# Performance work log

Measured on AMD Instinct MI355X. Metric: run time of the kernel, lower is better.

## Reference

```python
import jax, jax.numpy as jnp
import numpy as np

N_NODES = 100000
N_EDGES = 1600000
IN_DIM, HID, OUT_DIM = 128, 128, 64


def _glorot(key, fan_in, fan_out):
    s = float(np.sqrt(6.0 / (fan_in + fan_out)))
    return jax.random.uniform(key, (fan_in, fan_out), jnp.float32, -s, s)


def setup_inputs() -> dict:
    key = jax.random.key(0)
    ks = jax.random.split(key, 6)
    x = jax.random.normal(ks[0], (N_NODES, IN_DIM), jnp.float32)
    edge_index = jax.random.randint(ks[1], (2, N_EDGES), 0, N_NODES, jnp.int32)
    return {
        "x": x,
        "edge_index": edge_index,
        "W0": _glorot(ks[2], IN_DIM, HID), "b0": jnp.zeros((HID,), jnp.float32),
        "W1": _glorot(ks[3], HID, HID),    "b1": jnp.zeros((HID,), jnp.float32),
        "W2": _glorot(ks[4], HID, OUT_DIM), "b2": jnp.zeros((OUT_DIM,), jnp.float32),
    }


def _gcn_conv(x, src, dst, norm, W, b):
    # x' = D^{-1/2} (A+I) D^{-1/2} X W + b  (PyG GCNConv, add_self_loops=True)
    h = x @ W                       # [N, F_out]
    msg = h[src] * norm[:, None]    # [E+N, F_out] gathered, normalized messages
    out = jax.ops.segment_sum(msg, dst, num_segments=x.shape[0])
    return out + b


def reference(x, edge_index, W0, b0, W1, b1, W2, b2):
    n = x.shape[0]
    loop = jnp.arange(n, dtype=edge_index.dtype)
    src = jnp.concatenate([edge_index[0], loop])  # self-loops appended
    dst = jnp.concatenate([edge_index[1], loop])
    deg = jax.ops.segment_sum(jnp.ones_like(src, jnp.float32), dst, num_segments=n)
    dis = jnp.where(deg > 0, jax.lax.rsqrt(jnp.maximum(deg, 1e-12)), 0.0)
    norm = dis[src] * dis[dst]      # symmetric GCN normalization per edge

    h = jax.nn.relu(_gcn_conv(x, src, dst, norm, W0, b0))
    h = jax.nn.relu(_gcn_conv(h, src, dst, norm, W1, b1))
    h = jax.nn.relu(_gcn_conv(h, src, dst, norm, W2, b2))
    return jax.nn.log_softmax(h, axis=1)
```

## Files before the change

kernel.cpp:

```cpp
#include <hip/hip_runtime.h>

#define NN 100000
#define NE 1600000
#define NBK 782
#define NBLK 256
#define CHUNK ((NE + NBLK - 1) / NBLK)

typedef __bf16 bf16x4 __attribute__((ext_vector_type(4)));
typedef __bf16 bf16x8 __attribute__((ext_vector_type(8)));
typedef float f32x2 __attribute__((ext_vector_type(2)));
typedef float f32x4 __attribute__((ext_vector_type(4)));

#define ACC8_FP8(vv)                                                                  \
  {                                                                                   \
    f32x2 p;                                                                          \
    p = __builtin_amdgcn_cvt_pk_f32_fp8((vv).x, 0); acc[0] += p[0]; acc[1] += p[1];   \
    p = __builtin_amdgcn_cvt_pk_f32_fp8((vv).x, 1); acc[2] += p[0]; acc[3] += p[1];   \
    p = __builtin_amdgcn_cvt_pk_f32_fp8((vv).y, 0); acc[4] += p[0]; acc[5] += p[1];   \
    p = __builtin_amdgcn_cvt_pk_f32_fp8((vv).y, 1); acc[6] += p[0]; acc[7] += p[1];   \
  }


__global__ __launch_bounds__(256) void kW_prep(const float* __restrict__ W0, const float* __restrict__ W1,
                                               const float* __restrict__ W2, __bf16* __restrict__ Wt) {
  int i = blockIdx.x * 256 + threadIdx.x;
  if (i < 16384) {
    int k = i >> 7, n = i & 127;
    Wt[n * 128 + k] = (__bf16)W0[i];
  } else if (i < 32768) {
    int j = i - 16384;
    int k = j >> 7, n = j & 127;
    Wt[16384 + n * 128 + k] = (__bf16)W1[j];
  } else if (i < 40960) {
    int j = i - 32768;
    int k = j >> 6, n = j & 63;
    Wt[32768 + n * 128 + k] = (__bf16)W2[j];
  }
}


__global__ __launch_bounds__(256) void k1_hist(const int* __restrict__ dst, int* __restrict__ bhist) {
  __shared__ int h[NBK];
  int tid = threadIdx.x, b = blockIdx.x;
  for (int i = tid; i < NBK; i += 256) h[i] = 0;
  __syncthreads();
  int base = b * CHUNK, end = min(base + CHUNK, NE);
  for (int e = base + tid; e < end; e += 256) atomicAdd(&h[dst[e] >> 7], 1);
  __syncthreads();
  for (int i = tid; i < NBK; i += 256) bhist[i * NBLK + b] = h[i];
}

__global__ __launch_bounds__(256) void kA2(const int* __restrict__ bhist, int* __restrict__ btot) {
  int w = threadIdx.x >> 6, lane = threadIdx.x & 63;
  int bin = blockIdx.x * 4 + w;
  if (bin >= NBK) return;
  int4 v = *(const int4*)(bhist + bin * NBLK + lane * 4);
  int s = v.x + v.y + v.z + v.w;
#pragma unroll
  for (int off = 32; off > 0; off >>= 1) s += __shfl_xor(s, off);
  if (lane == 0) btot[bin] = s;
}

__global__ __launch_bounds__(1024) void kB_bscan(const int* __restrict__ btot, int* __restrict__ bptr) {
  __shared__ int s[1024];
  int tid = threadIdx.x;
  int v = (tid < NBK) ? btot[tid] : 0;
  s[tid] = v;
  __syncthreads();
  for (int off = 1; off < 1024; off <<= 1) {
    int t = (tid >= off) ? s[tid - off] : 0;
    __syncthreads();
    s[tid] += t;
    __syncthreads();
  }
  if (tid < NBK) bptr[tid + 1] = s[tid];
  if (tid == 0) bptr[0] = 0;
}

__global__ __launch_bounds__(256) void kC2(const int* __restrict__ bhist, const int* __restrict__ bptr,
                                           int* __restrict__ blockbase) {
  int w = threadIdx.x >> 6, lane = threadIdx.x & 63;
  int bin = blockIdx.x * 4 + w;
  if (bin >= NBK) return;
  int4 v = *(const int4*)(bhist + bin * NBLK + lane * 4);
  int ls = v.x + v.y + v.z + v.w;
  int incl = ls;
#pragma unroll
  for (int off = 1; off < 64; off <<= 1) {
    int t = __shfl_up(incl, off);
    if (lane >= off) incl += t;
  }
  int base = bptr[bin] + incl - ls;
  int4 o;
  o.x = base;
  o.y = base + v.x;
  o.z = base + v.x + v.y;
  o.w = base + v.x + v.y + v.z;
  *(int4*)(blockbase + bin * NBLK + lane * 4) = o;
}

__global__ __launch_bounds__(256) void k3_scatter(const int* __restrict__ src, const int* __restrict__ dst,
                                                  const int* __restrict__ blockbase, int* __restrict__ bucketed) {
  __shared__ int cur[NBK];
  int tid = threadIdx.x, b = blockIdx.x;
  for (int i = tid; i < NBK; i += 256) cur[i] = blockbase[i * NBLK + b];
  __syncthreads();
  int base = b * CHUNK, end = min(base + CHUNK, NE);
  for (int e = base + tid; e < end; e += 256) {
    int d = dst[e];
    int pos = atomicAdd(&cur[d >> 7], 1);
    bucketed[pos] = (src[e] << 7) | (d & 127);
  }
}

__global__ __launch_bounds__(256) void k_degfill(const int* __restrict__ bucketed, const int* __restrict__ bptr,
                                                 int* __restrict__ row_ptr, float* __restrict__ dis,
                                                 int* __restrict__ csr_src) {
  __shared__ int deg[128];
  __shared__ int sc[128];
  __shared__ int cur[128];
  int b = blockIdx.x, tid = threadIdx.x;
  int nb0 = b << 7;
  if (tid < 128) deg[tid] = 0;
  __syncthreads();
  int beg = bptr[b], end = bptr[b + 1];
  for (int e = beg + tid; e < end; e += 256) atomicAdd(&deg[bucketed[e] & 127], 1);
  __syncthreads();
  if (tid < 128) sc[tid] = deg[tid];
  __syncthreads();
  for (int off = 1; off < 128; off <<= 1) {
    int t = (tid >= off && tid < 128) ? sc[tid - off] : 0;
    __syncthreads();
    if (tid < 128) sc[tid] += t;
    __syncthreads();
  }
  if (tid < 128) {
    cur[tid] = beg + sc[tid] - deg[tid];
    if (nb0 + tid < NN) {
      row_ptr[nb0 + tid + 1] = beg + sc[tid];
      dis[nb0 + tid] = rsqrtf((float)(deg[tid] + 1));
      if (b == 0 && tid == 0) row_ptr[0] = 0;
    }
  }
  __syncthreads();
  for (int e = beg + tid; e < end; e += 256) {
    int pk = bucketed[e];
    int pos = atomicAdd(&cur[pk & 127], 1);
    csr_src[pos] = pk >> 7;
  }
}


template <int BN, int MODE, bool OUT8>
__global__ __launch_bounds__(256) void k_gemm(const void* __restrict__ Av, const __bf16* __restrict__ Wt,
                                              const float* __restrict__ bias, const float* __restrict__ dis,
                                              void* __restrict__ outv) {
  constexpr int LDK = 136;
  constexpr int NT = BN / 32;
  constexpr int ROWB = BN * (OUT8 ? 1 : 2);
  __shared__ __bf16 lB[BN * LDK];

  const int tid = threadIdx.x;
  const int rowBase = blockIdx.x * 128;
  const int lane = tid & 63;
  const int wid = tid >> 6;
  const int wm = (wid & 1) * 64;
  const int wn = (wid >> 1) * (BN / 2);
  const int lm = lane & 15;
  const int kg = lane >> 4;

  if (blockIdx.x == 0 && tid < ROWB / 16) {
    ((uint4*)((char*)outv + (size_t)NN * ROWB))[tid] = make_uint4(0, 0, 0, 0);
  }

  for (int c = tid; c < 16 * BN; c += 256) {
    int n = c >> 4;
    int koff = (c & 15) * 8;
    bf16x8 w = *(const bf16x8*)(Wt + n * 128 + koff);
    *(bf16x8*)&lB[n * LDK + koff] = w;
  }
  __syncthreads();

  f32x4 acc[4][NT] = {};
  const bool full = (rowBase + 128 <= NN);

#pragma unroll 2
  for (int ks = 0; ks < 128; ks += 32) {
    int k0 = ks + kg * 8;
    bf16x8 af[4];
    if constexpr (MODE == 0) {
      const float* A = (const float*)Av;
#pragma unroll
      for (int tm = 0; tm < 4; ++tm) {
        int gr = rowBase + wm + tm * 16 + lm;
        f32x4 a0 = {}, a1 = {};
        if (full || gr < NN) {
          a0 = *(const f32x4*)(A + (size_t)gr * 128 + k0);
          a1 = *(const f32x4*)(A + (size_t)gr * 128 + k0 + 4);
        }
        af[tm] = bf16x8{(__bf16)a0[0], (__bf16)a0[1], (__bf16)a0[2], (__bf16)a0[3],
                        (__bf16)a1[0], (__bf16)a1[1], (__bf16)a1[2], (__bf16)a1[3]};
      }
    } else {
      const __bf16* A = (const __bf16*)Av;
      f32x4 b0 = *(const f32x4*)(bias + k0);
      f32x4 b1 = *(const f32x4*)(bias + k0 + 4);
#pragma unroll
      for (int tm = 0; tm < 4; ++tm) {
        int gr = rowBase + wm + tm * 16 + lm;
        bf16x8 v = {};
        if (full || gr < NN) v = *(const bf16x8*)(A + (size_t)gr * 128 + k0);
        af[tm] = bf16x8{(__bf16)fmaxf((float)v[0] + b0[0], 0.f), (__bf16)fmaxf((float)v[1] + b0[1], 0.f),
                        (__bf16)fmaxf((float)v[2] + b0[2], 0.f), (__bf16)fmaxf((float)v[3] + b0[3], 0.f),
                        (__bf16)fmaxf((float)v[4] + b1[0], 0.f), (__bf16)fmaxf((float)v[5] + b1[1], 0.f),
                        (__bf16)fmaxf((float)v[6] + b1[2], 0.f), (__bf16)fmaxf((float)v[7] + b1[3], 0.f)};
      }
    }
    bf16x8 bfr[NT];
#pragma unroll
    for (int tn = 0; tn < NT; ++tn)
      bfr[tn] = *(const bf16x8*)&lB[(wn + tn * 16 + lm) * LDK + k0];
#pragma unroll
    for (int tm = 0; tm < 4; ++tm)
#pragma unroll
      for (int tn = 0; tn < NT; ++tn)
        acc[tm][tn] = __builtin_amdgcn_mfma_f32_16x16x32_bf16(af[tm], bfr[tn], acc[tm][tn], 0, 0, 0);
  }

#pragma unroll
  for (int tm = 0; tm < 4; ++tm) {
    int r0 = rowBase + wm + tm * 16 + kg * 4;
#pragma unroll
    for (int tn = 0; tn < NT; ++tn) {
      int c0 = wn + tn * 16 + lm;
#pragma unroll
      for (int r = 0; r < 4; ++r) {
        int gr = r0 + r;
        if (full || gr < NN) {
          float val = acc[tm][tn][r] * dis[gr];
          if constexpr (OUT8) {
            unsigned char* o8 = (unsigned char*)outv;
            unsigned pk = __builtin_amdgcn_cvt_pk_fp8_f32(val, val, 0, 0);
            o8[(size_t)gr * BN + c0] = (unsigned char)(pk & 0xffu);
          } else {
            __bf16* ob = (__bf16*)outv;
            ob[(size_t)gr * BN + c0] = (__bf16)val;
          }
        }
      }
    }
  }
}


__global__ __launch_bounds__(256) void k_agg128(const unsigned char* __restrict__ tmp8, const int* __restrict__ row_ptr,
                                                const int* __restrict__ csr_src, const float* __restrict__ dis,
                                                __bf16* __restrict__ agg) {
  int wid = (blockIdx.x * 256 + threadIdx.x) >> 6;
  int lane = threadIdx.x & 63;
  if (wid >= NN) return;
  int grp = lane >> 4;
  int fl = lane & 15;

  int beg = row_ptr[wid];
  int end = row_ptr[wid + 1];

  float acc[8] = {0.f, 0.f, 0.f, 0.f, 0.f, 0.f, 0.f, 0.f};
  if (grp == 0) {
    uint2 sv = *(const uint2*)(tmp8 + (size_t)wid * 128 + fl * 8);
    ACC8_FP8(sv);
  }

  for (int base = beg; base < end; base += 64) {
    int cnt = min(64, end - base);
    int sidx = (base + lane < end) ? csr_src[base + lane] : NN;
    int i = 0;
    while (i < cnt) {
      int rem = cnt - i;
      if (rem > 16) {
        uint2 v[8];
#pragma unroll
        for (int u = 0; u < 8; ++u) {
          int s = __shfl(sidx, (i + u * 4 + grp) & 63);
          v[u] = *(const uint2*)(tmp8 + (size_t)s * 128 + fl * 8);
        }
#pragma unroll
        for (int u = 0; u < 8; ++u) ACC8_FP8(v[u]);
        i += 32;
      } else {
        uint2 v[4];
#pragma unroll
        for (int u = 0; u < 4; ++u) {
          int s = __shfl(sidx, (i + u * 4 + grp) & 63);
          v[u] = *(const uint2*)(tmp8 + (size_t)s * 128 + fl * 8);
        }
#pragma unroll
        for (int u = 0; u < 4; ++u) ACC8_FP8(v[u]);
        i += 16;
      }
    }
  }

#pragma unroll
  for (int t = 0; t < 8; ++t) acc[t] += __shfl_xor(acc[t], 16);
#pragma unroll
  for (int t = 0; t < 8; ++t) acc[t] += __shfl_xor(acc[t], 32);

  if (grp == 0) {
    float d = dis[wid];
    bf16x8 o;
#pragma unroll
    for (int t = 0; t < 8; ++t) o[t] = (__bf16)(acc[t] * d);
    *(bf16x8*)&agg[(size_t)wid * 128 + fl * 8] = o;
  }
}


__global__ __launch_bounds__(256) void k_agg64_final(const __bf16* __restrict__ tmp, const int* __restrict__ row_ptr,
                                                     const int* __restrict__ csr_src, const float* __restrict__ dis,
                                                     const float* __restrict__ b2, float* __restrict__ out) {
  int wid = (blockIdx.x * 256 + threadIdx.x) >> 6;
  int lane = threadIdx.x & 63;
  int grp = lane >> 4;
  int fl = lane & 15;

  int beg = row_ptr[wid];
  int end = row_ptr[wid + 1];

  float acc[4] = {0.f, 0.f, 0.f, 0.f};
  if (grp == 0) {
    bf16x4 sv = *(const bf16x4*)&tmp[(size_t)wid * 64 + fl * 4];
#pragma unroll
    for (int t = 0; t < 4; ++t) acc[t] = (float)sv[t];
  }

  for (int base = beg; base < end; base += 64) {
    int cnt = min(64, end - base);
    int sidx = (base + lane < end) ? csr_src[base + lane] : NN;
    int i = 0;
    while (i < cnt) {
      int rem = cnt - i;
      if (rem > 16) {
        bf16x4 v[8];
#pragma unroll
        for (int u = 0; u < 8; ++u) {
          int s = __shfl(sidx, (i + u * 4 + grp) & 63);
          v[u] = *(const bf16x4*)&tmp[(size_t)s * 64 + fl * 4];
        }
#pragma unroll
        for (int u = 0; u < 8; ++u)
#pragma unroll
          for (int t = 0; t < 4; ++t) acc[t] += (float)v[u][t];
        i += 32;
      } else {
        bf16x4 v[4];
#pragma unroll
        for (int u = 0; u < 4; ++u) {
          int s = __shfl(sidx, (i + u * 4 + grp) & 63);
          v[u] = *(const bf16x4*)&tmp[(size_t)s * 64 + fl * 4];
        }
#pragma unroll
        for (int u = 0; u < 4; ++u)
#pragma unroll
          for (int t = 0; t < 4; ++t) acc[t] += (float)v[u][t];
        i += 16;
      }
    }
  }

#pragma unroll
  for (int t = 0; t < 4; ++t) acc[t] += __shfl_xor(acc[t], 16);
#pragma unroll
  for (int t = 0; t < 4; ++t) acc[t] += __shfl_xor(acc[t], 32);

  float d = dis[wid];
  float v[4], lm = -1e30f;
#pragma unroll
  for (int t = 0; t < 4; ++t) {
    v[t] = fmaxf(acc[t] * d + b2[fl * 4 + t], 0.f);
    lm = fmaxf(lm, v[t]);
  }
#pragma unroll
  for (int off = 8; off > 0; off >>= 1) lm = fmaxf(lm, __shfl_xor(lm, off));
  float le = 0.f;
#pragma unroll
  for (int t = 0; t < 4; ++t) le += __expf(v[t] - lm);
#pragma unroll
  for (int off = 8; off > 0; off >>= 1) le += __shfl_xor(le, off);
  float ls = lm + __logf(le);
  if (grp == 0) {
    f32x4 o = {v[0] - ls, v[1] - ls, v[2] - ls, v[3] - ls};
    *(f32x4*)&out[(size_t)wid * 64 + fl * 4] = o;
  }
}


extern "C" void kernel_launch(void* const* d_in, const int* in_sizes, int n_in,
                              void* d_out, int out_size, void* d_ws, size_t ws_size,
                              hipStream_t stream) {
  const float* x  = (const float*)d_in[0];
  const int*   ei = (const int*)d_in[1];
  const float* W0 = (const float*)d_in[2];
  const float* b0 = (const float*)d_in[3];
  const float* W1 = (const float*)d_in[4];
  const float* b1 = (const float*)d_in[5];
  const float* W2 = (const float*)d_in[6];
  const float* b2 = (const float*)d_in[7];
  const int* esrc = ei;
  const int* edst = ei + NE;

  char* p = (char*)d_ws;
  auto alloc = [&](size_t bytes) {
    char* q = p;
    p += (bytes + 255) & ~(size_t)255;
    return q;
  };
  float*  dis     = (float*)alloc((size_t)NN * 4);
  int*    row_ptr = (int*)alloc((size_t)(NN + 1) * 4);
  int*    btot    = (int*)alloc(NBK * 4);
  int*    bptr    = (int*)alloc((NBK + 1) * 4);
  __bf16* Wt      = (__bf16*)alloc(40960 * 2);
  int*    csr_src = (int*)alloc((size_t)NE * 4);
  char*   tmp     = (char*)alloc((size_t)(NN + 1) * 128 * 2);
  unsigned char* tmp8 = (unsigned char*)tmp;
  __bf16* tmp16   = (__bf16*)tmp;
  int*    bucketed  = (int*)tmp;
  int*    bhist     = csr_src;
  int*    blockbase = csr_src + NBLK * NBK;

  kW_prep<<<160, 256, 0, stream>>>(W0, W1, W2, Wt);
  k1_hist<<<NBLK, 256, 0, stream>>>(edst, bhist);
  kA2<<<(NBK + 3) / 4, 256, 0, stream>>>(bhist, btot);
  kB_bscan<<<1, 1024, 0, stream>>>(btot, bptr);
  kC2<<<(NBK + 3) / 4, 256, 0, stream>>>(bhist, bptr, blockbase);
  k3_scatter<<<NBLK, 256, 0, stream>>>(esrc, edst, blockbase, bucketed);
  k_degfill<<<NBK, 256, 0, stream>>>(bucketed, bptr, row_ptr, dis, csr_src);

  int gblocks = (NN + 127) / 128;
  int ablocks = (NN * 64 + 255) / 256;

  k_gemm<128, 0, true><<<gblocks, 256, 0, stream>>>(x, Wt, nullptr, dis, tmp8);
  k_agg128<<<ablocks, 256, 0, stream>>>(tmp8, row_ptr, csr_src, dis, (__bf16*)d_out);

  k_gemm<128, 2, true><<<gblocks, 256, 0, stream>>>(d_out, Wt + 16384, b0, dis, tmp8);
  k_agg128<<<ablocks, 256, 0, stream>>>(tmp8, row_ptr, csr_src, dis, (__bf16*)d_out);

  k_gemm<64, 2, false><<<gblocks, 256, 0, stream>>>(d_out, Wt + 32768, b1, dis, tmp16);
  k_agg64_final<<<ablocks, 256, 0, stream>>>(tmp16, row_ptr, csr_src, dis, b2, (float*)d_out);
}
```

Baseline: 364.0 us.

## Map four nodes per wavefront in aggregation, fuse weight prep, use warp-shuffle scan

The aggregation kernels now give each 16-lane group of a wavefront its own destination node instead of spreading one node's edges across four groups. This removes the cross-group shuffle reductions and launches a quarter as many blocks. The cost is that every group in a wavefront loops to the largest degree among its four nodes, so lanes go idle when degrees differ. Weight transposition is folded into extra blocks of the histogram kernel to save a launch, and the block-offset scan now uses wave shuffles instead of a barrier-heavy shared-memory scan.

```diff
diff --git a/kernel.cpp b/kernel.cpp
--- a/kernel.cpp
+++ b/kernel.cpp
@@ -21,27 +21,28 @@
   }
 
 
-__global__ __launch_bounds__(256) void kW_prep(const float* __restrict__ W0, const float* __restrict__ W1,
+__global__ __launch_bounds__(256) void k1_hist(const int* __restrict__ dst, int* __restrict__ bhist,
+                                               const float* __restrict__ W0, const float* __restrict__ W1,
                                                const float* __restrict__ W2, __bf16* __restrict__ Wt) {
-  int i = blockIdx.x * 256 + threadIdx.x;
-  if (i < 16384) {
-    int k = i >> 7, n = i & 127;
-    Wt[n * 128 + k] = (__bf16)W0[i];
-  } else if (i < 32768) {
-    int j = i - 16384;
-    int k = j >> 7, n = j & 127;
-    Wt[16384 + n * 128 + k] = (__bf16)W1[j];
-  } else if (i < 40960) {
-    int j = i - 32768;
-    int k = j >> 6, n = j & 63;
-    Wt[32768 + n * 128 + k] = (__bf16)W2[j];
-  }
-}
-
-
-__global__ __launch_bounds__(256) void k1_hist(const int* __restrict__ dst, int* __restrict__ bhist) {
+  int b = blockIdx.x;
+  if (b >= NBLK) {
+    int i = (b - NBLK) * 256 + threadIdx.x;
+    if (i < 16384) {
+      int k = i >> 7, n = i & 127;
+      Wt[n * 128 + k] = (__bf16)W0[i];
+    } else if (i < 32768) {
+      int j = i - 16384;
+      int k = j >> 7, n = j & 127;
+      Wt[16384 + n * 128 + k] = (__bf16)W1[j];
+    } else if (i < 40960) {
+      int j = i - 32768;
+      int k = j >> 6, n = j & 63;
+      Wt[32768 + n * 128 + k] = (__bf16)W2[j];
+    }
+    return;
+  }
   __shared__ int h[NBK];
-  int tid = threadIdx.x, b = blockIdx.x;
+  int tid = threadIdx.x;
   for (int i = tid; i < NBK; i += 256) h[i] = 0;
   __syncthreads();
   int base = b * CHUNK, end = min(base + CHUNK, NE);
@@ -62,18 +63,29 @@
 }
 
 __global__ __launch_bounds__(1024) void kB_bscan(const int* __restrict__ btot, int* __restrict__ bptr) {
-  __shared__ int s[1024];
-  int tid = threadIdx.x;
+  __shared__ int ws[16];
+  int tid = threadIdx.x, lane = tid & 63, w = tid >> 6;
   int v = (tid < NBK) ? btot[tid] : 0;
-  s[tid] = v;
-  __syncthreads();
-  for (int off = 1; off < 1024; off <<= 1) {
-    int t = (tid >= off) ? s[tid - off] : 0;
-    __syncthreads();
-    s[tid] += t;
-    __syncthreads();
-  }
-  if (tid < NBK) bptr[tid + 1] = s[tid];
+  int incl = v;
+#pragma unroll
+  for (int off = 1; off < 64; off <<= 1) {
+    int t = __shfl_up(incl, off);
+    if (lane >= off) incl += t;
+  }
+  if (lane == 63) ws[w] = incl;
+  __syncthreads();
+  if (tid < 16) {
+    int s = ws[tid];
+    int si = s;
+#pragma unroll
+    for (int off = 1; off < 16; off <<= 1) {
+      int t = __shfl_up(si, off);
+      if (lane >= off) si += t;
+    }
+    ws[tid] = si - s;
+  }
+  __syncthreads();
+  if (tid < NBK) bptr[tid + 1] = incl + ws[w];
   if (tid == 0) bptr[0] = 0;
 }
 
@@ -256,142 +268,129 @@
 __global__ __launch_bounds__(256) void k_agg128(const unsigned char* __restrict__ tmp8, const int* __restrict__ row_ptr,
                                                 const int* __restrict__ csr_src, const float* __restrict__ dis,
                                                 __bf16* __restrict__ agg) {
-  int wid = (blockIdx.x * 256 + threadIdx.x) >> 6;
+  int qw = (blockIdx.x * 256 + threadIdx.x) >> 6;
   int lane = threadIdx.x & 63;
-  if (wid >= NN) return;
-  int grp = lane >> 4;
+  int g = lane >> 4;
   int fl = lane & 15;
-
-  int beg = row_ptr[wid];
-  int end = row_ptr[wid + 1];
-
-  float acc[8] = {0.f, 0.f, 0.f, 0.f, 0.f, 0.f, 0.f, 0.f};
-  if (grp == 0) {
-    uint2 sv = *(const uint2*)(tmp8 + (size_t)wid * 128 + fl * 8);
+  int node = qw * 4 + g;
+
+  int beg = row_ptr[node];
+  int end = row_ptr[node + 1];
+
+  int mx = end - beg;
+  mx = max(mx, __shfl_xor(mx, 16));
+  mx = max(mx, __shfl_xor(mx, 32));
+
+  float acc[8] = {};
+  {
+    uint2 sv = *(const uint2*)(tmp8 + (size_t)node * 128 + fl * 8);
     ACC8_FP8(sv);
   }
 
-  for (int base = beg; base < end; base += 64) {
-    int cnt = min(64, end - base);
-    int sidx = (base + lane < end) ? csr_src[base + lane] : NN;
-    int i = 0;
-    while (i < cnt) {
-      int rem = cnt - i;
-      if (rem > 16) {
-        uint2 v[8];
-#pragma unroll
-        for (int u = 0; u < 8; ++u) {
-          int s = __shfl(sidx, (i + u * 4 + grp) & 63);
-          v[u] = *(const uint2*)(tmp8 + (size_t)s * 128 + fl * 8);
-        }
-#pragma unroll
-        for (int u = 0; u < 8; ++u) ACC8_FP8(v[u]);
-        i += 32;
-      } else {
-        uint2 v[4];
-#pragma unroll
-        for (int u = 0; u < 4; ++u) {
-          int s = __shfl(sidx, (i + u * 4 + grp) & 63);
-          v[u] = *(const uint2*)(tmp8 + (size_t)s * 128 + fl * 8);
-        }
-#pragma unroll
-        for (int u = 0; u < 4; ++u) ACC8_FP8(v[u]);
-        i += 16;
-      }
-    }
-  }
-
-#pragma unroll
-  for (int t = 0; t < 8; ++t) acc[t] += __shfl_xor(acc[t], 16);
-#pragma unroll
-  for (int t = 0; t < 8; ++t) acc[t] += __shfl_xor(acc[t], 32);
-
-  if (grp == 0) {
-    float d = dis[wid];
-    bf16x8 o;
-#pragma unroll
-    for (int t = 0; t < 8; ++t) o[t] = (__bf16)(acc[t] * d);
-    *(bf16x8*)&agg[(size_t)wid * 128 + fl * 8] = o;
-  }
+  for (int done = 0; done < mx; done += 16) {
+    int ep = beg + done + fl;
+    int sidx = (ep < end) ? csr_src[ep] : NN;
+    int rem = mx - done;
+    {
+      uint2 v[8];
+#pragma unroll
+      for (int u = 0; u < 8; ++u) {
+        int s = __shfl(sidx, g * 16 + u);
+        v[u] = *(const uint2*)(tmp8 + (size_t)s * 128 + fl * 8);
+      }
+#pragma unroll
+      for (int u = 0; u < 8; ++u) ACC8_FP8(v[u]);
+    }
+    if (rem > 8) {
+      uint2 v[8];
+#pragma unroll
+      for (int u = 0; u < 8; ++u) {
+        int s = __shfl(sidx, g * 16 + 8 + u);
+        v[u] = *(const uint2*)(tmp8 + (size_t)s * 128 + fl * 8);
+      }
+#pragma unroll
+      for (int u = 0; u < 8; ++u) ACC8_FP8(v[u]);
+    }
+  }
+
+  float d = dis[node];
+  bf16x8 o;
+#pragma unroll
+  for (int t = 0; t < 8; ++t) o[t] = (__bf16)(acc[t] * d);
+  *(bf16x8*)&agg[(size_t)node * 128 + fl * 8] = o;
 }
 
 
 __global__ __launch_bounds__(256) void k_agg64_final(const __bf16* __restrict__ tmp, const int* __restrict__ row_ptr,
                                                      const int* __restrict__ csr_src, const float* __restrict__ dis,
                                                      const float* __restrict__ b2, float* __restrict__ out) {
-  int wid = (blockIdx.x * 256 + threadIdx.x) >> 6;
+  int qw = (blockIdx.x * 256 + threadIdx.x) >> 6;
   int lane = threadIdx.x & 63;
-  int grp = lane >> 4;
+  int g = lane >> 4;
   int fl = lane & 15;
-
-  int beg = row_ptr[wid];
-  int end = row_ptr[wid + 1];
-
-  float acc[4] = {0.f, 0.f, 0.f, 0.f};
-  if (grp == 0) {
-    bf16x4 sv = *(const bf16x4*)&tmp[(size_t)wid * 64 + fl * 4];
+  int node = qw * 4 + g;
+
+  int beg = row_ptr[node];
+  int end = row_ptr[node + 1];
+
+  int mx = end - beg;
+  mx = max(mx, __shfl_xor(mx, 16));
+  mx = max(mx, __shfl_xor(mx, 32));
+
+  float acc[4] = {};
+  {
+    bf16x4 sv = *(const bf16x4*)&tmp[(size_t)node * 64 + fl * 4];
 #pragma unroll
     for (int t = 0; t < 4; ++t) acc[t] = (float)sv[t];
   }
 
-  for (int base = beg; base < end; base += 64) {
-    int cnt = min(64, end - base);
-    int sidx = (base + lane < end) ? csr_src[base + lane] : NN;
-    int i = 0;
-    while (i < cnt) {
-      int rem = cnt - i;
-      if (rem > 16) {
-        bf16x4 v[8];
-#pragma unroll
-        for (int u = 0; u < 8; ++u) {
-          int s = __shfl(sidx, (i + u * 4 + grp) & 63);
-          v[u] = *(const bf16x4*)&tmp[(size_t)s * 64 + fl * 4];
-        }
-#pragma unroll
-        for (int u = 0; u < 8; ++u)
-#pragma unroll
-          for (int t = 0; t < 4; ++t) acc[t] += (float)v[u][t];
-        i += 32;
-      } else {
-        bf16x4 v[4];
-#pragma unroll
-        for (int u = 0; u < 4; ++u) {
-          int s = __shfl(sidx, (i + u * 4 + grp) & 63);
-          v[u] = *(const bf16x4*)&tmp[(size_t)s * 64 + fl * 4];
-        }
-#pragma unroll
-        for (int u = 0; u < 4; ++u)
-#pragma unroll
-          for (int t = 0; t < 4; ++t) acc[t] += (float)v[u][t];
-        i += 16;
-      }
-    }
-  }
-
-#pragma unroll
-  for (int t = 0; t < 4; ++t) acc[t] += __shfl_xor(acc[t], 16);
-#pragma unroll
-  for (int t = 0; t < 4; ++t) acc[t] += __shfl_xor(acc[t], 32);
-
-  float d = dis[wid];
-  float v[4], lm = -1e30f;
+  for (int done = 0; done < mx; done += 16) {
+    int ep = beg + done + fl;
+    int sidx = (ep < end) ? csr_src[ep] : NN;
+    int rem = mx - done;
+    {
+      bf16x4 v[8];
+#pragma unroll
+      for (int u = 0; u < 8; ++u) {
+        int s = __shfl(sidx, g * 16 + u);
+        v[u] = *(const bf16x4*)&tmp[(size_t)s * 64 + fl * 4];
+      }
+#pragma unroll
+      for (int u = 0; u < 8; ++u)
+#pragma unroll
+        for (int t = 0; t < 4; ++t) acc[t] += (float)v[u][t];
+    }
+    if (rem > 8) {
+      bf16x4 v[8];
+#pragma unroll
+      for (int u = 0; u < 8; ++u) {
+        int s = __shfl(sidx, g * 16 + 8 + u);
+        v[u] = *(const bf16x4*)&tmp[(size_t)s * 64 + fl * 4];
+      }
+#pragma unroll
+      for (int u = 0; u < 8; ++u)
+#pragma unroll
+        for (int t = 0; t < 4; ++t) acc[t] += (float)v[u][t];
+    }
+  }
+
+  float d = dis[node];
+  float v4[4], lm = -1e30f;
 #pragma unroll
   for (int t = 0; t < 4; ++t) {
-    v[t] = fmaxf(acc[t] * d + b2[fl * 4 + t], 0.f);
-    lm = fmaxf(lm, v[t]);
+    v4[t] = fmaxf(acc[t] * d + b2[fl * 4 + t], 0.f);
+    lm = fmaxf(lm, v4[t]);
   }
 #pragma unroll
   for (int off = 8; off > 0; off >>= 1) lm = fmaxf(lm, __shfl_xor(lm, off));
   float le = 0.f;
 #pragma unroll
-  for (int t = 0; t < 4; ++t) le += __expf(v[t] - lm);
+  for (int t = 0; t < 4; ++t) le += __expf(v4[t] - lm);
 #pragma unroll
   for (int off = 8; off > 0; off >>= 1) le += __shfl_xor(le, off);
   float ls = lm + __logf(le);
-  if (grp == 0) {
-    f32x4 o = {v[0] - ls, v[1] - ls, v[2] - ls, v[3] - ls};
-    *(f32x4*)&out[(size_t)wid * 64 + fl * 4] = o;
-  }
+  f32x4 o = {v4[0] - ls, v4[1] - ls, v4[2] - ls, v4[3] - ls};
+  *(f32x4*)&out[(size_t)node * 64 + fl * 4] = o;
 }
 
 
@@ -428,8 +427,7 @@
   int*    bhist     = csr_src;
   int*    blockbase = csr_src + NBLK * NBK;
 
-  kW_prep<<<160, 256, 0, stream>>>(W0, W1, W2, Wt);
-  k1_hist<<<NBLK, 256, 0, stream>>>(edst, bhist);
+  k1_hist<<<NBLK + 160, 256, 0, stream>>>(edst, bhist, W0, W1, W2, Wt);
   kA2<<<(NBK + 3) / 4, 256, 0, stream>>>(bhist, btot);
   kB_bscan<<<1, 1024, 0, stream>>>(btot, bptr);
   kC2<<<(NBK + 3) / 4, 256, 0, stream>>>(bhist, bptr, blockbase);
@@ -437,7 +435,7 @@
   k_degfill<<<NBK, 256, 0, stream>>>(bucketed, bptr, row_ptr, dis, csr_src);
 
   int gblocks = (NN + 127) / 128;
-  int ablocks = (NN * 64 + 255) / 256;
+  int ablocks = NN / 16;
 
   k_gemm<128, 0, true><<<gblocks, 256, 0, stream>>>(x, Wt, nullptr, dis, tmp8);
   k_agg128<<<ablocks, 256, 0, stream>>>(tmp8, row_ptr, csr_src, dis, (__bf16*)d_out);
```

Result: faster. 336.7 us (-7.5%).
